# Kernel tuning notes

Measured on AMD Instinct MI355X. Metric: run time of the kernel, lower is better.

## Reference

```python
import jax, jax.numpy as jnp
import numpy as np

B, S, D, H = 2, 2048, 1024, 16
HD = D // H
SCALE = HD ** -0.5
NEG = -1e30


def setup_inputs() -> dict:
    key = jax.random.key(0)
    ks = jax.random.split(key, 10)
    w = lambda k: jax.random.normal(k, (D, D), dtype=jnp.float32) * 0.02
    b = lambda k: jax.random.normal(k, (D,), dtype=jnp.float32) * 0.01
    hidden_states = jax.random.normal(ks[0], (B, S, D), dtype=jnp.float32)
    document_ids = jnp.sort(jax.random.randint(ks[1], (S,), 0, 16))
    return {
        'hidden_states': hidden_states,
        'wq': w(ks[2]), 'bq': b(ks[3]),
        'wk': w(ks[4]), 'bk': b(ks[5]),
        'wv': w(ks[6]), 'bv': b(ks[7]),
        'wo': w(ks[8]), 'bo': b(ks[9]),
        'document_ids': document_ids,
    }


def reference(hidden_states, wq, bq, wk, bk, wv, bv, wo, bo, document_ids):
    # projections (nn.Linear: x @ W.T + b)
    q = (hidden_states @ wq.T + bq).reshape(B, S, H, HD)
    k = (hidden_states @ wk.T + bk).reshape(B, S, H, HD)
    v = (hidden_states @ wv.T + bv).reshape(B, S, H, HD)
    # document-block mask: attend only within same document
    mask = document_ids[:, None] == document_ids[None, :]  # [S, S]
    scores = jnp.einsum('bqhd,bkhd->bhqk', q, k) * SCALE
    scores = jnp.where(mask[None, None], scores, NEG)
    attn = jax.nn.softmax(scores, axis=-1)
    out = jnp.einsum('bhqk,bkhd->bqhd', attn, v).reshape(B, S, D)
    return out @ wo.T + bo
```

## Files before the change

kernel.cpp:

```cpp
#include <hip/hip_runtime.h>
#include <hip/hip_bf16.h>
#include <math.h>

#define B 2
#define S 2048
#define D 1024
#define H 16
#define HD 64
#define SCALE 0.125f
#define NEGBIG -1e30f

#define NE 4194304
#define NW 1048576
#define NE8 524288
#define NW8 131072

typedef _Float16 f16;
typedef _Float16 f16x8 __attribute__((ext_vector_type(8)));
typedef _Float16 f16x4 __attribute__((ext_vector_type(4)));
typedef float f32x4  __attribute__((ext_vector_type(4)));

__device__ __forceinline__ void gl_lds16(const void* g, void* l) {
    __builtin_amdgcn_global_load_lds(
        (const __attribute__((address_space(1))) unsigned int*)g,
        (__attribute__((address_space(3))) unsigned int*)l, 16, 0, 0);
}

__device__ __forceinline__ void wave_lds_fence() {
    __builtin_amdgcn_wave_barrier();
    __builtin_amdgcn_s_waitcnt(0xC07F);
    __builtin_amdgcn_wave_barrier();
}

__global__ __launch_bounds__(256) void prep_k(
    const float4* __restrict__ hs,
    const float4* __restrict__ wq, const float4* __restrict__ wk,
    const float4* __restrict__ wv, const float4* __restrict__ wo,
    const int* __restrict__ doc,
    f16x8* __restrict__ xh, f16x8* __restrict__ wqkv, f16x8* __restrict__ woh,
    int* __restrict__ dstart, int* __restrict__ dend)
{
    int i = blockIdx.x * blockDim.x + threadIdx.x;
    if (i < NE8 + 4 * NW8) {
        const float4* src;
        f16x8* dst;
        if (i < NE8) { src = hs + 2 * (size_t)i; dst = xh + i; }
        else {
            int j = i - NE8;
            int id = j / NW8, jj = j - id * NW8;
            src = ((id == 0) ? wq : (id == 1) ? wk : (id == 2) ? wv : wo) + 2 * (size_t)jj;
            dst = (id < 3) ? (wqkv + (size_t)id * NW8 + jj) : (woh + jj);
        }
        float4 a = src[0], b = src[1];
        f16x8 h;
        h[0] = (f16)a.x; h[1] = (f16)a.y; h[2] = (f16)a.z; h[3] = (f16)a.w;
        h[4] = (f16)b.x; h[5] = (f16)b.y; h[6] = (f16)b.z; h[7] = (f16)b.w;
        *dst = h;
    } else {
        int s = i - (NE8 + 4 * NW8);
        if (s < S) {
            int v = doc[s];
            int lo = 0, hi = S;
            while (lo < hi) { int mid = (lo + hi) >> 1; if (doc[mid] < v) lo = mid + 1; else hi = mid; }
            dstart[s] = lo;
            lo = 0; hi = S;
            while (lo < hi) { int mid = (lo + hi) >> 1; if (doc[mid] <= v) lo = mid + 1; else hi = mid; }
            dend[s] = lo;
        }
    }
}

__global__ __launch_bounds__(512, 2) void qkv_mfma_k(
    const f16* __restrict__ xh, const f16* __restrict__ wqkv,
    const float* __restrict__ bq, const float* __restrict__ bk,
    const float* __restrict__ bv,
    f16* __restrict__ Qh, f16* __restrict__ Kh, f16* __restrict__ Vth)
{
    __shared__ union {
        struct { f16 At[2][256 * 64]; f16 Bt[2][256 * 64]; } s;
        f16 tr[64 * 264];
    } lds;

    const int which = blockIdx.z;
    const f16* Bg = wqkv + (size_t)which * D * D;

    const int tid = threadIdx.x;
    const int w = tid >> 6, ln = tid & 63;
    const int wm = (w & 1) * 128, wn = (w >> 1) * 64;
    const int lc = ln & 15, quad = ln >> 4;
    const int m0 = blockIdx.y * 256, n0 = blockIdx.x * 256;

    size_t aoff[4], boff[4];
    int ldst[4];
    #pragma unroll
    for (int i = 0; i < 4; i++) {
        int r = w * 32 + i * 8 + (ln >> 3);
        int o = (ln & 7) ^ (r & 7);
        aoff[i] = (size_t)(m0 + r) * 1024 + o * 8;
        boff[i] = (size_t)(n0 + r) * 1024 + o * 8;
        ldst[i] = (w * 32 + i * 8) * 64;
    }

    f32x4 acc[8][4];
    #pragma unroll
    for (int i = 0; i < 8; i++)
        #pragma unroll
        for (int j = 0; j < 4; j++) acc[i][j] = (f32x4){0.f, 0.f, 0.f, 0.f};

    #define STAGE(buf, k0) { \
        f16* Ad_ = lds.s.At[buf]; f16* Bd_ = lds.s.Bt[buf]; \
        _Pragma("unroll") \
        for (int i_ = 0; i_ < 4; i_++) gl_lds16(xh + aoff[i_] + (k0), Ad_ + ldst[i_]); \
        _Pragma("unroll") \
        for (int i_ = 0; i_ < 4; i_++) gl_lds16(Bg + boff[i_] + (k0), Bd_ + ldst[i_]); }

    STAGE(0, 0)
    STAGE(1, 64)
    asm volatile("s_waitcnt vmcnt(8)");
    __builtin_amdgcn_sched_barrier(0);
    __builtin_amdgcn_s_barrier();
    __builtin_amdgcn_sched_barrier(0);

    for (int kt = 0; kt < 16; ++kt) {
        const int cur = kt & 1;
        const f16* Acur = lds.s.At[cur];
        const f16* Bcur = lds.s.Bt[cur];

        #pragma unroll
        for (int q = 0; q < 4; ++q) {
            f16x8 af[2][2], bf[4][2];
            #pragma unroll
            for (int t = 0; t < 2; t++) {
                int am = wm + (q * 2 + t) * 16 + lc;
                #pragma unroll
                for (int ks = 0; ks < 2; ks++)
                    af[t][ks] = *(const f16x8*)&Acur[am * 64 + (((ks * 4 + quad) ^ (am & 7)) * 8)];
            }
            #pragma unroll
            for (int t = 0; t < 4; t++) {
                int bn = wn + t * 16 + lc;
                #pragma unroll
                for (int ks = 0; ks < 2; ks++)
                    bf[t][ks] = *(const f16x8*)&Bcur[bn * 64 + (((ks * 4 + quad) ^ (bn & 7)) * 8)];
            }
            __builtin_amdgcn_s_setprio(1);
            #pragma unroll
            for (int ks = 0; ks < 2; ks++)
                #pragma unroll
                for (int mt = 0; mt < 2; mt++)
                    #pragma unroll
                    for (int nt = 0; nt < 4; nt++)
                        acc[q * 2 + mt][nt] = __builtin_amdgcn_mfma_f32_16x16x32_f16(
                            af[mt][ks], bf[nt][ks], acc[q * 2 + mt][nt], 0, 0, 0);
            __builtin_amdgcn_s_setprio(0);
        }

        if (kt == 15) break;

        __builtin_amdgcn_s_barrier();
        __builtin_amdgcn_sched_barrier(0);
        if (kt + 2 < 16) {
            STAGE(cur, (kt + 2) * 64)
            asm volatile("s_waitcnt vmcnt(8)");
        } else {
            asm volatile("s_waitcnt vmcnt(0)");
        }
        __builtin_amdgcn_sched_barrier(0);
        __builtin_amdgcn_s_barrier();
        __builtin_amdgcn_sched_barrier(0);
    }
    #undef STAGE

    if (which < 2) {
        const float* bias = (which == 0) ? bq : bk;
        f16* dst = (which == 0) ? Qh : Kh;
        #pragma unroll
        for (int nt = 0; nt < 4; nt++) {
            int col = n0 + wn + nt * 16 + lc;
            float bias_v = bias[col];
            int h = col >> 6, hd = col & 63;
            #pragma unroll
            for (int mt = 0; mt < 8; mt++) {
                #pragma unroll
                for (int r = 0; r < 4; r++) {
                    int m = m0 + wm + mt * 16 + quad * 4 + r;
                    int bbm = m >> 11, s = m & (S - 1);
                    float val = acc[mt][nt][r] + bias_v;
                    if (which == 0) val *= SCALE;
                    size_t idx = (((size_t)(bbm * H + h) * S) + s) * HD + hd;
                    dst[idx] = (f16)val;
                }
            }
        }
    } else {
        const int bb = m0 >> 11;
        const int sbase = m0 & (S - 1);
        __syncthreads();
        #pragma unroll
        for (int pass = 0; pass < 4; pass++) {
            if ((w >> 1) == pass) {
                #pragma unroll
                for (int nt = 0; nt < 4; nt++) {
                    int colp = nt * 16 + lc;
                    float bvv = bv[n0 + pass * 64 + colp];
                    #pragma unroll
                    for (int mt = 0; mt < 8; mt++) {
                        f16x4 v;
                        #pragma unroll
                        for (int r = 0; r < 4; r++) v[r] = (f16)(acc[mt][nt][r] + bvv);
                        *(f16x4*)&lds.tr[colp * 264 + wm + mt * 16 + quad * 4] = v;
                    }
                }
            }
            __syncthreads();
            #pragma unroll
            for (int p2 = 0; p2 < 4; p2++) {
                int chunk = tid + p2 * 512;
                int colp = chunk >> 5;
                int oct = chunk & 31;
                f16x8 v = *(const f16x8*)&lds.tr[colp * 264 + oct * 8];
                int vcol = n0 + pass * 64 + colp;
                int h = vcol >> 6, hd = vcol & 63;
                size_t idx = (((size_t)(bb * H + h) * HD) + hd) * S + sbase + oct * 8;
                *(f16x8*)(Vth + idx) = v;
            }
            __syncthreads();
        }
    }
}

__global__ __launch_bounds__(256) void out_mfma_k(
    const f16* __restrict__ oh, const f16* __restrict__ wh,
    const float* __restrict__ bias, float* __restrict__ Y)
{
    __shared__ f16 Ah[128 * 64], Bh[64 * 64];
    const int tid = threadIdx.x;
    const int w = tid >> 6, ln = tid & 63;
    const int wm = (w & 1) * 64, wn = (w >> 1) * 32;
    const int lc = ln & 15, quad = ln >> 4;
    const int m0 = blockIdx.y * 128, n0 = blockIdx.x * 64;

    f32x4 acc[4][2];
    #pragma unroll
    for (int i = 0; i < 4; i++)
        #pragma unroll
        for (int j = 0; j < 2; j++) acc[i][j] = (f32x4){0.f, 0.f, 0.f, 0.f};

    for (int k0 = 0; k0 < 1024; k0 += 64) {
        #pragma unroll
        for (int i = 0; i < 4; i++) {
            int rl = w * 32 + i * 8 + (ln >> 3);
            int oc = (ln & 7) ^ (rl & 7);
            gl_lds16(oh + (size_t)(m0 + rl) * 1024 + k0 + oc * 8, Ah + (w * 32 + i * 8) * 64);
        }
        #pragma unroll
        for (int i = 0; i < 2; i++) {
            int rl = w * 16 + i * 8 + (ln >> 3);
            int oc = (ln & 7) ^ (rl & 7);
            gl_lds16(wh + (size_t)(n0 + rl) * 1024 + k0 + oc * 8, Bh + (w * 16 + i * 8) * 64);
        }
        __syncthreads();

        #pragma unroll
        for (int ks = 0; ks < 2; ks++) {
            f16x8 ah[4], bh[2];
            #pragma unroll
            for (int t = 0; t < 4; t++) {
                int am = wm + t * 16 + lc;
                ah[t] = *(const f16x8*)&Ah[am * 64 + (((ks * 4 + quad) ^ (am & 7)) * 8)];
            }
            #pragma unroll
            for (int t = 0; t < 2; t++) {
                int bn = wn + t * 16 + lc;
                bh[t] = *(const f16x8*)&Bh[bn * 64 + (((ks * 4 + quad) ^ (bn & 7)) * 8)];
            }
            #pragma unroll
            for (int mt = 0; mt < 4; mt++)
                #pragma unroll
                for (int nt = 0; nt < 2; nt++)
                    acc[mt][nt] = __builtin_amdgcn_mfma_f32_16x16x32_f16(ah[mt], bh[nt], acc[mt][nt], 0, 0, 0);
        }
        __syncthreads();
    }

    #pragma unroll
    for (int nt = 0; nt < 2; nt++) {
        int col = n0 + wn + nt * 16 + lc;
        float bv_ = bias[col];
        #pragma unroll
        for (int mt = 0; mt < 4; mt++) {
            #pragma unroll
            for (int r = 0; r < 4; r++) {
                int m = m0 + wm + mt * 16 + quad * 4 + r;
                Y[(size_t)m * D + col] = acc[mt][nt][r] + bv_;
            }
        }
    }
}

__device__ __forceinline__ void load_kfrag(
    const f16* __restrict__ Kh, size_t bh, int j0, int lc, int quad, f16x8 kf[4][2])
{
    #pragma unroll
    for (int t = 0; t < 4; t++) {
        size_t krow = (bh + j0 + t * 16 + lc) * HD;
        #pragma unroll
        for (int ks = 0; ks < 2; ks++)
            kf[t][ks] = *(const f16x8*)(Kh + krow + ks * 32 + quad * 8);
    }
}

__global__ __launch_bounds__(256) void attn4_k(
    const f16* __restrict__ Qh, const f16* __restrict__ Kh,
    const f16* __restrict__ Vth,
    const int* __restrict__ dstart, const int* __restrict__ dend,
    f16* __restrict__ Ohi)
{
    const int qt = blockIdx.x, h = blockIdx.y, b = blockIdx.z;
    const int tid = threadIdx.x;
    const int w = tid >> 6, ln = tid & 63;
    const int lc = ln & 15, quad = ln >> 4;
    const int q0 = qt * 64 + w * 16;
    const size_t bh  = ((size_t)b * H + h) * S;
    const size_t bhv = ((size_t)b * H + h) * HD;

    __shared__ float Ps[4][2][16 * 65];

    int row_st[4], row_en[4];
    #pragma unroll
    for (int r = 0; r < 4; r++) {
        row_st[r] = dstart[q0 + quad * 4 + r];
        row_en[r] = dend[q0 + quad * 4 + r];
    }
    const int kstart = dstart[q0] & ~63;
    const int kend   = dend[q0 + 15];

    const size_t qrow = bh + q0 + lc;
    f16x8 qf[2];
    #pragma unroll
    for (int ks = 0; ks < 2; ks++)
        qf[ks] = *(const f16x8*)(Qh + qrow * HD + ks * 32 + quad * 8);

    f32x4 o[4];
    #pragma unroll
    for (int nt = 0; nt < 4; nt++) o[nt] = (f32x4){0.f, 0.f, 0.f, 0.f};
    f32x4 m_i = (f32x4){NEGBIG, NEGBIG, NEGBIG, NEGBIG};
    f32x4 l_i = (f32x4){0.f, 0.f, 0.f, 0.f};

    f16x8 kf[4][2], kf2[4][2];
    load_kfrag(Kh, bh, kstart, lc, quad, kf);

    int it = 0;
    for (int j0 = kstart; j0 < kend; j0 += 64, it ^= 1) {
        float* ps = &Ps[w][it][0];
        const bool more = (j0 + 64) < kend;
        if (more) load_kfrag(Kh, bh, j0 + 64, lc, quad, kf2);

        f32x4 sc[4];
        #pragma unroll
        for (int t = 0; t < 4; t++) {
            f32x4 a = (f32x4){0.f, 0.f, 0.f, 0.f};
            #pragma unroll
            for (int ks = 0; ks < 2; ks++)
                a = __builtin_amdgcn_mfma_f32_16x16x32_f16(qf[ks], kf[t][ks], a, 0, 0, 0);
            int key = j0 + t * 16 + lc;
            #pragma unroll
            for (int r = 0; r < 4; r++) {
                bool valid = (key >= row_st[r]) && (key < row_en[r]);
                sc[t][r] = valid ? a[r] : NEGBIG;
            }
        }

        f32x4 mx = sc[0];
        #pragma unroll
        for (int t = 1; t < 4; t++)
            #pragma unroll
            for (int r = 0; r < 4; r++) mx[r] = fmaxf(mx[r], sc[t][r]);
        #pragma unroll
        for (int off = 1; off <= 8; off <<= 1)
            #pragma unroll
            for (int r = 0; r < 4; r++) mx[r] = fmaxf(mx[r], __shfl_xor(mx[r], off, 64));

        f32x4 m_new, alpha;
        #pragma unroll
        for (int r = 0; r < 4; r++) {
            m_new[r] = fmaxf(m_i[r], mx[r]);
            alpha[r] = __expf(m_i[r] - m_new[r]);
        }

        f32x4 psum = (f32x4){0.f, 0.f, 0.f, 0.f};
        f32x4 pv[4];
        #pragma unroll
        for (int t = 0; t < 4; t++) {
            #pragma unroll
            for (int r = 0; r < 4; r++) {
                float p = __expf(sc[t][r] - m_new[r]);
                p = (sc[t][r] < -5e29f) ? 0.f : p;
                pv[t][r] = p;
                psum[r] += p;
            }
        }
        #pragma unroll
        for (int off = 1; off <= 8; off <<= 1)
            #pragma unroll
            for (int r = 0; r < 4; r++) psum[r] += __shfl_xor(psum[r], off, 64);

        #pragma unroll
        for (int r = 0; r < 4; r++) {
            l_i[r] = l_i[r] * alpha[r] + psum[r];
            m_i[r] = m_new[r];
        }
        #pragma unroll
        for (int nt = 0; nt < 4; nt++)
            #pragma unroll
            for (int r = 0; r < 4; r++) o[nt][r] *= alpha[r];

        f16x8 vh[2][4];
        #pragma unroll
        for (int ks = 0; ks < 2; ks++) {
            int gp = ks * 4 + quad;
            #pragma unroll
            for (int nt = 0; nt < 4; nt++) {
                int dim = nt * 16 + lc;
                vh[ks][nt] = *(const f16x8*)(Vth + (bhv + dim) * S + j0 + gp * 8);
            }
        }

        #pragma unroll
        for (int t = 0; t < 4; t++) {
            int g = 2 * t + (lc >> 3);
            #pragma unroll
            for (int r = 0; r < 4; r++) {
                int q = quad * 4 + r;
                ps[q * 65 + ((g ^ (q & 7)) * 8) + (lc & 7)] = pv[t][r];
            }
        }

        wave_lds_fence();

        #pragma unroll
        for (int ks = 0; ks < 2; ks++) {
            int gp = ks * 4 + quad;
            const float* prow = &ps[lc * 65 + ((gp ^ (lc & 7)) * 8)];
            f16x8 ph;
            #pragma unroll
            for (int j = 0; j < 8; j++) ph[j] = (f16)prow[j];
            #pragma unroll
            for (int nt = 0; nt < 4; nt++)
                o[nt] = __builtin_amdgcn_mfma_f32_16x16x32_f16(ph, vh[ks][nt], o[nt], 0, 0, 0);
        }

        if (more) {
            #pragma unroll
            for (int t = 0; t < 4; t++)
                #pragma unroll
                for (int ks = 0; ks < 2; ks++) kf[t][ks] = kf2[t][ks];
        }
    }

    f32x4 inv;
    #pragma unroll
    for (int r = 0; r < 4; r++) inv[r] = 1.f / l_i[r];
    #pragma unroll
    for (int nt = 0; nt < 4; nt++) {
        int dim = nt * 16 + lc;
        #pragma unroll
        for (int r = 0; r < 4; r++) {
            int q = q0 + quad * 4 + r;
            float val = o[nt][r] * inv[r];
            size_t idx = ((size_t)(b * S + q)) * D + h * 64 + dim;
            Ohi[idx] = (f16)val;
        }
    }
}

extern "C" void kernel_launch(void* const* d_in, const int* in_sizes, int n_in,
                              void* d_out, int out_size, void* d_ws, size_t ws_size,
                              hipStream_t stream) {
    const float* hs = (const float*)d_in[0];
    const float* wq = (const float*)d_in[1];
    const float* bq = (const float*)d_in[2];
    const float* wk = (const float*)d_in[3];
    const float* bk = (const float*)d_in[4];
    const float* wv = (const float*)d_in[5];
    const float* bv = (const float*)d_in[6];
    const float* wo = (const float*)d_in[7];
    const float* bo = (const float*)d_in[8];
    const int*  doc = (const int*)d_in[9];
    float* out = (float*)d_out;

    f16* xh   = (f16*)d_ws;
    f16* Qhb  = xh + NE;
    f16* Khb  = Qhb + NE;
    f16* Vth  = Khb + NE;
    f16* wqkv = Vth + NE;
    f16* woh  = wqkv + 3 * (size_t)NW;
    int* dstart = (int*)(woh + NW);
    int* dend = dstart + S;

    prep_k<<<(NE8 + 4 * NW8 + S + 255) / 256, 256, 0, stream>>>(
        (const float4*)hs, (const float4*)wq, (const float4*)wk,
        (const float4*)wv, (const float4*)wo, doc,
        (f16x8*)xh, (f16x8*)wqkv, (f16x8*)woh, dstart, dend);

    qkv_mfma_k<<<dim3(D / 256, (B * S) / 256, 3), 512, 0, stream>>>(
        xh, wqkv, bq, bk, bv, Qhb, Khb, Vth);
    attn4_k<<<dim3(S / 64, H, B), 256, 0, stream>>>(
        Qhb, Khb, Vth, dstart, dend, xh);
    out_mfma_k<<<dim3(D / 64, (B * S) / 128), 256, 0, stream>>>(xh, woh, bo, out);
}
```

Before: 187.9 us.

## Interleave QKV GEMM global loads with MFMA quarters and swizzle block order

The QKV projection GEMM main loop is restructured into four phases per k-tile. Each phase issues a subset of the next tiles' global-to-LDS loads, then runs a quarter of the MFMAs between barriers, rather than loading a whole stage in one burst. The 3D grid is also flattened to 192 blocks with an XCD-aware swizzle of block index to (which, m, n), to improve L2 locality across the chiplets. The extra barriers per k-tile and the fine-grained vmcnt bookkeeping add synchronization overhead and risk of ordering errors.

Result: faster. 183.2 us (-2.5%).

```diff
diff --git a/kernel.cpp b/kernel.cpp
--- a/kernel.cpp
+++ b/kernel.cpp
@@ -81,25 +81,26 @@
         f16 tr[64 * 264];
     } lds;
 
-    const int which = blockIdx.z;
+    const int l = blockIdx.x;
+    const int swz = (l & 7) * 24 + (l >> 3);
+    const int which = swz >> 6;
+    const int r2 = swz & 63;
+    const int m0 = (r2 >> 2) * 256, n0 = (r2 & 3) * 256;
     const f16* Bg = wqkv + (size_t)which * D * D;
 
     const int tid = threadIdx.x;
     const int w = tid >> 6, ln = tid & 63;
     const int wm = (w & 1) * 128, wn = (w >> 1) * 64;
     const int lc = ln & 15, quad = ln >> 4;
-    const int m0 = blockIdx.y * 256, n0 = blockIdx.x * 256;
-
-    size_t aoff[4], boff[4];
-    int ldst[4];
-    #pragma unroll
-    for (int i = 0; i < 4; i++) {
-        int r = w * 32 + i * 8 + (ln >> 3);
-        int o = (ln & 7) ^ (r & 7);
-        aoff[i] = (size_t)(m0 + r) * 1024 + o * 8;
-        boff[i] = (size_t)(n0 + r) * 1024 + o * 8;
-        ldst[i] = (w * 32 + i * 8) * 64;
-    }
+
+    const int srow = w * 8 + (ln >> 3);
+    const int soct = (ln & 7) ^ (srow & 7);
+    const size_t aBase = (size_t)(m0 + srow) * 1024 + soct * 8;
+    const size_t bBase = (size_t)(n0 + srow) * 1024 + soct * 8;
+    const int lBase = w * 512;
+
+#define UA(u, kt, buf) gl_lds16(xh + aBase + (size_t)(u) * 65536 + (kt) * 64, lds.s.At[buf] + (u) * 4096 + lBase)
+#define UB(u, kt, buf) gl_lds16(Bg + bBase + (size_t)(u) * 65536 + (kt) * 64, lds.s.Bt[buf] + (u) * 4096 + lBase)
 
     f32x4 acc[8][4];
     #pragma unroll
@@ -107,69 +108,85 @@
         #pragma unroll
         for (int j = 0; j < 4; j++) acc[i][j] = (f32x4){0.f, 0.f, 0.f, 0.f};
 
-    #define STAGE(buf, k0) { \
-        f16* Ad_ = lds.s.At[buf]; f16* Bd_ = lds.s.Bt[buf]; \
-        _Pragma("unroll") \
-        for (int i_ = 0; i_ < 4; i_++) gl_lds16(xh + aoff[i_] + (k0), Ad_ + ldst[i_]); \
-        _Pragma("unroll") \
-        for (int i_ = 0; i_ < 4; i_++) gl_lds16(Bg + boff[i_] + (k0), Bd_ + ldst[i_]); }
-
-    STAGE(0, 0)
-    STAGE(1, 64)
-    asm volatile("s_waitcnt vmcnt(8)");
+    UB(0, 0, 0); UB(1, 0, 0); UB(2, 0, 0); UB(3, 0, 0);
+    UA(0, 0, 0); UA(1, 0, 0); UA(2, 0, 0); UA(3, 0, 0);
+    UB(0, 1, 1); UB(1, 1, 1); UB(2, 1, 1); UA(0, 1, 1); UB(3, 1, 1); UA(2, 1, 1);
+    asm volatile("s_waitcnt vmcnt(6)");
     __builtin_amdgcn_sched_barrier(0);
     __builtin_amdgcn_s_barrier();
     __builtin_amdgcn_sched_barrier(0);
 
-    for (int kt = 0; kt < 16; ++kt) {
-        const int cur = kt & 1;
-        const f16* Acur = lds.s.At[cur];
-        const f16* Bcur = lds.s.Bt[cur];
-
-        #pragma unroll
-        for (int q = 0; q < 4; ++q) {
-            f16x8 af[2][2], bf[4][2];
-            #pragma unroll
-            for (int t = 0; t < 2; t++) {
-                int am = wm + (q * 2 + t) * 16 + lc;
-                #pragma unroll
-                for (int ks = 0; ks < 2; ks++)
-                    af[t][ks] = *(const f16x8*)&Acur[am * 64 + (((ks * 4 + quad) ^ (am & 7)) * 8)];
-            }
-            #pragma unroll
-            for (int t = 0; t < 4; t++) {
-                int bn = wn + t * 16 + lc;
-                #pragma unroll
-                for (int ks = 0; ks < 2; ks++)
-                    bf[t][ks] = *(const f16x8*)&Bcur[bn * 64 + (((ks * 4 + quad) ^ (bn & 7)) * 8)];
-            }
-            __builtin_amdgcn_s_setprio(1);
+#define READ_AF(q_, Ab_) { \
+    _Pragma("unroll") \
+    for (int tt = 0; tt < 2; tt++) { \
+        int am = wm + ((q_) * 2 + tt) * 16 + lc; \
+        _Pragma("unroll") \
+        for (int ks = 0; ks < 2; ks++) \
+            af[tt][ks] = *(const f16x8*)&Ab_[am * 64 + (((ks * 4 + quad) ^ (am & 7)) * 8)]; \
+    } }
+
+#define MFMA_Q(q_) { \
+    __builtin_amdgcn_s_setprio(1); \
+    _Pragma("unroll") \
+    for (int ks = 0; ks < 2; ks++) \
+        _Pragma("unroll") \
+        for (int mt = 0; mt < 2; mt++) \
+            _Pragma("unroll") \
+            for (int nt = 0; nt < 4; nt++) \
+                acc[(q_) * 2 + mt][nt] = __builtin_amdgcn_mfma_f32_16x16x32_f16( \
+                    af[mt][ks], bf[nt][ks], acc[(q_) * 2 + mt][nt], 0, 0, 0); \
+    __builtin_amdgcn_s_setprio(0); }
+
+#define BAR_IN() { \
+    __builtin_amdgcn_sched_barrier(0); \
+    __builtin_amdgcn_s_barrier(); \
+    asm volatile("s_waitcnt lgkmcnt(0)"); \
+    __builtin_amdgcn_sched_barrier(0); }
+
+#define BAR_OUT() { \
+    __builtin_amdgcn_sched_barrier(0); \
+    __builtin_amdgcn_s_barrier(); \
+    __builtin_amdgcn_sched_barrier(0); }
+
+    #pragma unroll 1
+    for (int t = 0; t < 16; ++t) {
+        const int cur = t & 1, nxt = cur ^ 1;
+        const f16* Ab = lds.s.At[cur];
+        const f16* Bb = lds.s.Bt[cur];
+        f16x8 af[2][2], bf[4][2];
+
+        #pragma unroll
+        for (int nt = 0; nt < 4; nt++) {
+            int bn = wn + nt * 16 + lc;
             #pragma unroll
             for (int ks = 0; ks < 2; ks++)
-                #pragma unroll
-                for (int mt = 0; mt < 2; mt++)
-                    #pragma unroll
-                    for (int nt = 0; nt < 4; nt++)
-                        acc[q * 2 + mt][nt] = __builtin_amdgcn_mfma_f32_16x16x32_f16(
-                            af[mt][ks], bf[nt][ks], acc[q * 2 + mt][nt], 0, 0, 0);
-            __builtin_amdgcn_s_setprio(0);
-        }
-
-        if (kt == 15) break;
-
-        __builtin_amdgcn_s_barrier();
-        __builtin_amdgcn_sched_barrier(0);
-        if (kt + 2 < 16) {
-            STAGE(cur, (kt + 2) * 64)
-            asm volatile("s_waitcnt vmcnt(8)");
-        } else {
-            asm volatile("s_waitcnt vmcnt(0)");
-        }
-        __builtin_amdgcn_sched_barrier(0);
-        __builtin_amdgcn_s_barrier();
-        __builtin_amdgcn_sched_barrier(0);
-    }
-    #undef STAGE
+                bf[nt][ks] = *(const f16x8*)&Bb[bn * 64 + (((ks * 4 + quad) ^ (bn & 7)) * 8)];
+        }
+        READ_AF(0, Ab)
+        if (t < 15) { UA(1, t + 1, nxt); UA(3, t + 1, nxt); }
+        BAR_IN(); MFMA_Q(0); BAR_OUT();
+
+        READ_AF(1, Ab)
+        if (t < 14) { UB(0, t + 2, cur); UB(1, t + 2, cur); }
+        BAR_IN(); MFMA_Q(1); BAR_OUT();
+
+        READ_AF(2, Ab)
+        if (t < 14) { UB(2, t + 2, cur); UA(0, t + 2, cur); }
+        BAR_IN(); MFMA_Q(2); BAR_OUT();
+
+        READ_AF(3, Ab)
+        if (t < 14) { UB(3, t + 2, cur); UA(2, t + 2, cur); }
+        BAR_IN(); MFMA_Q(3);
+        if (t < 14)       { asm volatile("s_waitcnt vmcnt(6)"); }
+        else if (t == 14) { asm volatile("s_waitcnt vmcnt(0)"); }
+        BAR_OUT();
+    }
+#undef UA
+#undef UB
+#undef READ_AF
+#undef MFMA_Q
+#undef BAR_IN
+#undef BAR_OUT
 
     if (which < 2) {
         const float* bias = (which == 0) ? bq : bk;
@@ -503,7 +520,7 @@
         (const float4*)wv, (const float4*)wo, doc,
         (f16x8*)xh, (f16x8*)wqkv, (f16x8*)woh, dstart, dend);
 
-    qkv_mfma_k<<<dim3(D / 256, (B * S) / 256, 3), 512, 0, stream>>>(
+    qkv_mfma_k<<<192, 512, 0, stream>>>(
         xh, wqkv, bq, bk, bv, Qhb, Khb, Vth);
     attn4_k<<<dim3(S / 64, H, B), 256, 0, stream>>>(
         Qhb, Khb, Vth, dstart, dend, xh);
```
